# Kernel optimization log

Measured on AMD Instinct MI355X. Metric: run time of the kernel, lower is better.

The kernel has to match this reference:

```python
import jax, jax.numpy as jnp
import numpy as np

# sign with straight-through estimator: grad passes only where |input| < 1
@jax.custom_vjp
def sign_ste(x):
    return jnp.sign(x)

def _sign_ste_fwd(x):
    return jnp.sign(x), x

def _sign_ste_bwd(x, g):
    return (jnp.where(jnp.abs(x) < 1.0, g, jnp.zeros_like(g)),)

sign_ste.defvjp(_sign_ste_fwd, _sign_ste_bwd)

# weight binarization: torch mutates weight.data in-place, so autograd treats
# sign() as identity w.r.t. the weight variable (plain linear gradient)
@jax.custom_vjp
def sign_id(w):
    return jnp.sign(w)

def _sign_id_fwd(w):
    return jnp.sign(w), None

def _sign_id_bwd(_, g):
    return (g,)

sign_id.defvjp(_sign_id_fwd, _sign_id_bwd)


def setup_inputs() -> dict:
    key = jax.random.key(0)
    k1, k2, k3 = jax.random.split(key, 3)
    x = jax.random.normal(k1, (8192, 4096), dtype=jnp.float32)
    # weight initialized to random ±1 (bernoulli(0.5)*2-1), as in __init__
    W = jnp.sign(jax.random.normal(k2, (4096, 4096), dtype=jnp.float32))
    b = jax.random.normal(k3, (4096,), dtype=jnp.float32) * 0.02
    return {"x": x, "W": W, "b": b}


def reference(x, W, b):
    # x: [N, in]; W: [out, in]; b: [out]
    x_mean = jnp.mean(jnp.abs(x))          # scalar scale, differentiable
    xb = sign_ste(x)                        # ±1 activations, STE gradient
    wb = sign_id(W)                         # ±1 weights, identity gradient
    out = jnp.einsum('ni,oi->no', xb, wb) + b  # [N, out]
    return out * x_mean
```

## Files before the change

### kernel.cpp

```cpp
#include <hip/hip_runtime.h>

typedef int intx4 __attribute__((ext_vector_type(4)));
typedef int intx8 __attribute__((ext_vector_type(8)));
typedef float floatx4 __attribute__((ext_vector_type(4)));

#define M_DIM 8192
#define N_DIM 4096
#define K_DIM 4096
#define KB2 (K_DIM / 2)

__device__ __forceinline__ void gld_lds16(const char* g, char* l) {
  __builtin_amdgcn_global_load_lds(
      (const __attribute__((address_space(1))) unsigned int*)g,
      (__attribute__((address_space(3))) unsigned int*)l,
      16, 0, 0);
}

__device__ __forceinline__ unsigned nib(float v) {
  return v > 0.0f ? 0x2u : (v < 0.0f ? 0xAu : 0x0u);
}

__device__ __forceinline__ float pack32(const float* __restrict__ src, int4* __restrict__ dst) {
  float s = 0.0f;
  int4 o;
  int* op = (int*)&o;
  #pragma unroll
  for (int q = 0; q < 4; ++q) {
    float4 v0 = ((const float4*)src)[2 * q];
    float4 v1 = ((const float4*)src)[2 * q + 1];
    op[q] = (int)(nib(v0.x) | (nib(v0.y) << 4) | (nib(v0.z) << 8) | (nib(v0.w) << 12) |
                  (nib(v1.x) << 16) | (nib(v1.y) << 20) | (nib(v1.z) << 24) | (nib(v1.w) << 28));
    s += fabsf(v0.x) + fabsf(v0.y) + fabsf(v0.z) + fabsf(v0.w)
       + fabsf(v1.x) + fabsf(v1.y) + fabsf(v1.z) + fabsf(v1.w);
  }
  *dst = o;
  return s;
}

__global__ __launch_bounds__(256) void pack_kernel(const float* __restrict__ x,
                                                   const float* __restrict__ Wm,
                                                   char* __restrict__ xb,
                                                   char* __restrict__ wb,
                                                   double* __restrict__ accd) {
  const int t = threadIdx.x;
  if (blockIdx.x < 2048) {
    const size_t nch = (size_t)M_DIM * K_DIM / 32;
    size_t tid = (size_t)blockIdx.x * 256 + t;
    float s = 0.0f;
    for (size_t c = tid; c < nch; c += (size_t)2048 * 256)
      s += pack32(x + c * 32, (int4*)(xb + c * 16));
    #pragma unroll
    for (int off = 32; off > 0; off >>= 1) s += __shfl_down(s, off);
    __shared__ float part[4];
    if ((t & 63) == 0) part[t >> 6] = s;
    __syncthreads();
    if (t == 0) atomicAdd(accd, (double)(part[0] + part[1] + part[2] + part[3]));
  } else {
    const size_t nch = (size_t)N_DIM * K_DIM / 32;
    size_t tid = (size_t)(blockIdx.x - 2048) * 256 + t;
    for (size_t c = tid; c < nch; c += (size_t)1024 * 256)
      pack32(Wm + c * 32, (int4*)(wb + c * 16));
  }
}

__global__ __launch_bounds__(256) void gemm_kernel(const char* __restrict__ Xb,
                                                   const char* __restrict__ Wb,
                                                   const float* __restrict__ bias,
                                                   const double* __restrict__ accd,
                                                   float* __restrict__ out) {
  __shared__ __align__(16) char ldsA[128 * 64];
  __shared__ __align__(16) char ldsB[128 * 64];
  const int t = threadIdx.x;
  const int lane = t & 63;
  const int w = t >> 6;
  const int m16 = lane & 15;
  const int quad = lane >> 4;
  const int bM = blockIdx.y * 128;
  const int bN = blockIdx.x * 128;
  const int waveM = (w & 1) * 64;
  const int waveN = (w >> 1) * 64;
  const int srl = 2 * (t >> 3) + (t & 1);
  const int ssc = (t >> 1) & 3;

  floatx4 acc[4][4];
  #pragma unroll
  for (int i = 0; i < 4; ++i)
    #pragma unroll
    for (int j = 0; j < 4; ++j)
      acc[i][j] = (floatx4){0.0f, 0.0f, 0.0f, 0.0f};

  for (int kt = 0; kt < K_DIM; kt += 128) {
    __syncthreads();
    #pragma unroll
    for (int rd = 0; rd < 2; ++rd) {
      const int r = rd * 64 + srl;
      const int g = (ssc + (r >> 1)) & 3;
      const size_t goff = (size_t)(kt >> 1) + g * 16;
      gld_lds16(Xb + (size_t)(bM + r) * KB2 + goff, ldsA + rd * 4096 + w * 1024);
      gld_lds16(Wb + (size_t)(bN + r) * KB2 + goff, ldsB + rd * 4096 + w * 1024);
    }
    __syncthreads();

    intx8 a8[4];
    #pragma unroll
    for (int i = 0; i < 4; ++i) {
      const int m = waveM + i * 16 + m16;
      const int c = (quad - (m >> 1)) & 3;
      intx4 lo = *(const intx4*)&ldsA[(m >> 1) * 128 + c * 32 + (m & 1) * 16];
      a8[i] = (intx8){lo[0], lo[1], lo[2], lo[3], 0, 0, 0, 0};
    }
    #pragma unroll
    for (int j = 0; j < 4; ++j) {
      const int n = waveN + j * 16 + m16;
      const int c = (quad - (n >> 1)) & 3;
      intx4 lo = *(const intx4*)&ldsB[(n >> 1) * 128 + c * 32 + (n & 1) * 16];
      intx8 b8 = (intx8){lo[0], lo[1], lo[2], lo[3], 0, 0, 0, 0};
      #pragma unroll
      for (int i = 0; i < 4; ++i)
        acc[i][j] = __builtin_amdgcn_mfma_scale_f32_16x16x128_f8f6f4(
            a8[i], b8, acc[i][j],
            4, 4,
            0, 0x7F7F7F7F,
            0, 0x7F7F7F7F);
    }
  }

  const float scale = (float)(*accd * (1.0 / (double)((size_t)M_DIM * K_DIM)));

  #pragma unroll
  for (int j = 0; j < 4; ++j) {
    const int col = bN + waveN + j * 16 + m16;
    const float bj = bias[col];
    #pragma unroll
    for (int i = 0; i < 4; ++i) {
      const size_t row0 = (size_t)(bM + waveM + i * 16 + quad * 4);
      float* po = out + row0 * N_DIM + col;
      #pragma unroll
      for (int r = 0; r < 4; ++r)
        po[(size_t)r * N_DIM] = (acc[i][j][r] + bj) * scale;
    }
  }
}

extern "C" void kernel_launch(void* const* d_in, const int* in_sizes, int n_in,
                              void* d_out, int out_size, void* d_ws, size_t ws_size,
                              hipStream_t stream) {
  const float* x = (const float*)d_in[0];
  const float* W = (const float*)d_in[1];
  const float* b = (const float*)d_in[2];
  float* out = (float*)d_out;

  double* accd = (double*)d_ws;
  char* Xb = (char*)d_ws + 256;
  char* Wb = (char*)d_ws + 256 + (size_t)M_DIM * K_DIM / 2;

  hipMemsetAsync(d_ws, 0, 8, stream);
  pack_kernel<<<3072, 256, 0, stream>>>(x, W, Xb, Wb, accd);
  gemm_kernel<<<dim3(N_DIM / 128, M_DIM / 128), 256, 0, stream>>>(Xb, Wb, b, accd, out);
}
```

Baseline: 351.8 us.

## Double-buffer GEMM LDS tiles, swizzle block order, and flatten pack kernel

The GEMM now uses two LDS buffers per operand, so the global-to-LDS load for the next K tile is issued while MFMAs run on the current one. This removes one barrier per iteration. Blocks are remapped through a 1D swizzle so that neighbouring blocks share M/N tiles for L2 reuse. The pack kernel is flattened into a single grid-stride loop where each thread handles one float4 and emits a 16-bit packed word, which relies on Xb and Wb being contiguous in the workspace. This costs narrower stores and a branch per element in exchange for simpler, coalesced indexing.

```diff
diff --git a/kernel.cpp b/kernel.cpp
--- a/kernel.cpp
+++ b/kernel.cpp
@@ -8,6 +8,10 @@
 #define N_DIM 4096
 #define K_DIM 4096
 #define KB2 (K_DIM / 2)
+
+#define PACK_BLOCKS 2048
+#define NF4_X ((size_t)M_DIM * K_DIM / 4)
+#define NF4_TOT (NF4_X + (size_t)N_DIM * K_DIM / 4)
 
 __device__ __forceinline__ void gld_lds16(const char* g, char* l) {
   __builtin_amdgcn_global_load_lds(
@@ -20,47 +24,32 @@
   return v > 0.0f ? 0x2u : (v < 0.0f ? 0xAu : 0x0u);
 }
 
-__device__ __forceinline__ float pack32(const float* __restrict__ src, int4* __restrict__ dst) {
-  float s = 0.0f;
-  int4 o;
-  int* op = (int*)&o;
-  #pragma unroll
-  for (int q = 0; q < 4; ++q) {
-    float4 v0 = ((const float4*)src)[2 * q];
-    float4 v1 = ((const float4*)src)[2 * q + 1];
-    op[q] = (int)(nib(v0.x) | (nib(v0.y) << 4) | (nib(v0.z) << 8) | (nib(v0.w) << 12) |
-                  (nib(v1.x) << 16) | (nib(v1.y) << 20) | (nib(v1.z) << 24) | (nib(v1.w) << 28));
-    s += fabsf(v0.x) + fabsf(v0.y) + fabsf(v0.z) + fabsf(v0.w)
-       + fabsf(v1.x) + fabsf(v1.y) + fabsf(v1.z) + fabsf(v1.w);
-  }
-  *dst = o;
-  return s;
-}
-
 __global__ __launch_bounds__(256) void pack_kernel(const float* __restrict__ x,
                                                    const float* __restrict__ Wm,
-                                                   char* __restrict__ xb,
-                                                   char* __restrict__ wb,
+                                                   unsigned short* __restrict__ pk,
                                                    double* __restrict__ accd) {
   const int t = threadIdx.x;
-  if (blockIdx.x < 2048) {
-    const size_t nch = (size_t)M_DIM * K_DIM / 32;
-    size_t tid = (size_t)blockIdx.x * 256 + t;
-    float s = 0.0f;
-    for (size_t c = tid; c < nch; c += (size_t)2048 * 256)
-      s += pack32(x + c * 32, (int4*)(xb + c * 16));
-    #pragma unroll
-    for (int off = 32; off > 0; off >>= 1) s += __shfl_down(s, off);
-    __shared__ float part[4];
-    if ((t & 63) == 0) part[t >> 6] = s;
-    __syncthreads();
-    if (t == 0) atomicAdd(accd, (double)(part[0] + part[1] + part[2] + part[3]));
-  } else {
-    const size_t nch = (size_t)N_DIM * K_DIM / 32;
-    size_t tid = (size_t)(blockIdx.x - 2048) * 256 + t;
-    for (size_t c = tid; c < nch; c += (size_t)1024 * 256)
-      pack32(Wm + c * 32, (int4*)(wb + c * 16));
+  const size_t stride = (size_t)PACK_BLOCKS * 256;
+  const float4* __restrict__ X4 = (const float4*)x;
+  const float4* __restrict__ W4 = (const float4*)Wm;
+  float s = 0.0f;
+  for (size_t i = (size_t)blockIdx.x * 256 + t; i < NF4_TOT; i += stride) {
+    float4 v;
+    if (i < NF4_X) {
+      v = X4[i];
+      s += fabsf(v.x) + fabsf(v.y) + fabsf(v.z) + fabsf(v.w);
+    } else {
+      v = W4[i - NF4_X];
+    }
+    pk[i] = (unsigned short)(nib(v.x) | (nib(v.y) << 4) | (nib(v.z) << 8) |
+                             (nib(v.w) << 12));
   }
+  #pragma unroll
+  for (int off = 32; off > 0; off >>= 1) s += __shfl_down(s, off);
+  __shared__ float sp[4];
+  if ((t & 63) == 0) sp[t >> 6] = s;
+  __syncthreads();
+  if (t == 0) atomicAdd(accd, (double)(sp[0] + sp[1] + sp[2] + sp[3]));
 }
 
 __global__ __launch_bounds__(256) void gemm_kernel(const char* __restrict__ Xb,
@@ -68,15 +57,19 @@
                                                    const float* __restrict__ bias,
                                                    const double* __restrict__ accd,
                                                    float* __restrict__ out) {
-  __shared__ __align__(16) char ldsA[128 * 64];
-  __shared__ __align__(16) char ldsB[128 * 64];
+  __shared__ __align__(16) char ldsA[2][128 * 64];
+  __shared__ __align__(16) char ldsB[2][128 * 64];
   const int t = threadIdx.x;
   const int lane = t & 63;
   const int w = t >> 6;
   const int m16 = lane & 15;
   const int quad = lane >> 4;
-  const int bM = blockIdx.y * 128;
-  const int bN = blockIdx.x * 128;
+
+  const int id = blockIdx.x;
+  const int swz = (id & 7) * 256 + (id >> 3);
+  const int bM = (swz >> 5) * 128;
+  const int bN = (swz & 31) * 128;
+
   const int waveM = (w & 1) * 64;
   const int waveN = (w >> 1) * 64;
   const int srl = 2 * (t >> 3) + (t & 1);
@@ -89,31 +82,38 @@
     for (int j = 0; j < 4; ++j)
       acc[i][j] = (floatx4){0.0f, 0.0f, 0.0f, 0.0f};
 
-  for (int kt = 0; kt < K_DIM; kt += 128) {
-    __syncthreads();
+  auto stage = [&](int ki, int buf) {
+    const size_t kb = (size_t)ki << 6;
     #pragma unroll
     for (int rd = 0; rd < 2; ++rd) {
       const int r = rd * 64 + srl;
       const int g = (ssc + (r >> 1)) & 3;
-      const size_t goff = (size_t)(kt >> 1) + g * 16;
-      gld_lds16(Xb + (size_t)(bM + r) * KB2 + goff, ldsA + rd * 4096 + w * 1024);
-      gld_lds16(Wb + (size_t)(bN + r) * KB2 + goff, ldsB + rd * 4096 + w * 1024);
+      const size_t goff = kb + (size_t)(g * 16);
+      gld_lds16(Xb + (size_t)(bM + r) * KB2 + goff, &ldsA[buf][rd * 4096 + w * 1024]);
+      gld_lds16(Wb + (size_t)(bN + r) * KB2 + goff, &ldsB[buf][rd * 4096 + w * 1024]);
     }
-    __syncthreads();
+  };
+
+  stage(0, 0);
+  __syncthreads();
+
+  for (int ki = 0; ki < K_DIM / 128; ++ki) {
+    const int cur = ki & 1;
+    if (ki + 1 < K_DIM / 128) stage(ki + 1, cur ^ 1);
 
     intx8 a8[4];
     #pragma unroll
     for (int i = 0; i < 4; ++i) {
       const int m = waveM + i * 16 + m16;
       const int c = (quad - (m >> 1)) & 3;
-      intx4 lo = *(const intx4*)&ldsA[(m >> 1) * 128 + c * 32 + (m & 1) * 16];
+      intx4 lo = *(const intx4*)&ldsA[cur][(m >> 1) * 128 + c * 32 + (m & 1) * 16];
       a8[i] = (intx8){lo[0], lo[1], lo[2], lo[3], 0, 0, 0, 0};
     }
     #pragma unroll
     for (int j = 0; j < 4; ++j) {
       const int n = waveN + j * 16 + m16;
       const int c = (quad - (n >> 1)) & 3;
-      intx4 lo = *(const intx4*)&ldsB[(n >> 1) * 128 + c * 32 + (n & 1) * 16];
+      intx4 lo = *(const intx4*)&ldsB[cur][(n >> 1) * 128 + c * 32 + (n & 1) * 16];
       intx8 b8 = (intx8){lo[0], lo[1], lo[2], lo[3], 0, 0, 0, 0};
       #pragma unroll
       for (int i = 0; i < 4; ++i)
@@ -123,6 +123,7 @@
             0, 0x7F7F7F7F,
             0, 0x7F7F7F7F);
     }
+    __syncthreads();
   }
 
   const float scale = (float)(*accd * (1.0 / (double)((size_t)M_DIM * K_DIM)));
@@ -155,6 +156,6 @@
   char* Wb = (char*)d_ws + 256 + (size_t)M_DIM * K_DIM / 2;
 
   hipMemsetAsync(d_ws, 0, 8, stream);
-  pack_kernel<<<3072, 256, 0, stream>>>(x, W, Xb, Wb, accd);
-  gemm_kernel<<<dim3(N_DIM / 128, M_DIM / 128), 256, 0, stream>>>(Xb, Wb, b, accd, out);
+  pack_kernel<<<PACK_BLOCKS, 256, 0, stream>>>(x, W, (unsigned short*)Xb, accd);
+  gemm_kernel<<<2048, 256, 0, stream>>>(Xb, Wb, b, accd, out);
 }
```

Result: slower. 375.6 us (+6.7%).
